# Kernel tuning notes

Measured on AMD Instinct MI355X. Metric: run time of the kernel, lower is better.

Reference implementation:

```python
import jax, jax.numpy as jnp
import numpy as np

D = 11           # num_classes + 1 (embedding dim)
HL = 7           # window height = 1 + 2*H_PAD
WL = 7           # window width  = 1 + 2*W_PAD
PAD = 3
MAXH, MAXW = 30, 30
FF = 64          # dim_feedforward
EPS = 1e-5       # LayerNorm eps (torch default)
PAD_VALUE = 0.0


def setup_inputs() -> dict:
    key = jax.random.key(0)
    ks = jax.random.split(key, 6)
    N, C, H, W = 1, 10, 16, 16
    s = 0.1
    return {
        "x": jax.random.uniform(ks[0], (N, C, H, W), jnp.float32),
        "Wqkv": jax.random.normal(ks[1], (3 * D, D), jnp.float32) * s,  # in_proj_weight
        "Wo": jax.random.normal(ks[2], (D, D), jnp.float32) * s,        # out_proj.weight
        "W1": jax.random.normal(ks[3], (FF, D), jnp.float32) * s,       # linear1.weight
        "W2": jax.random.normal(ks[4], (D, FF), jnp.float32) * s,       # linear2.weight
        "ln1_w": jnp.ones((D,), jnp.float32),                           # norm1.weight (bias=False)
        "ln2_w": jnp.ones((D,), jnp.float32),                           # norm2.weight (bias=False)
    }


def _layer_norm(x, w):
    m = jnp.mean(x, axis=-1, keepdims=True)
    v = jnp.mean(jnp.square(x - m), axis=-1, keepdims=True)
    return (x - m) / jnp.sqrt(v + EPS) * w


def _encoder_layer(x, Wqkv, Wo, W1, W2, ln1_w, ln2_w):
    # x: [B, S, D]; post-norm, 1 head, no biases, eval mode (dropout off)
    qkv = x @ Wqkv.T
    q, k, v = jnp.split(qkv, 3, axis=-1)
    scale = 1.0 / jnp.sqrt(jnp.float32(D))
    attn = jax.nn.softmax(jnp.einsum('bqd,bkd->bqk', q, k) * scale, axis=-1)
    sa = jnp.einsum('bqk,bkd->bqd', attn, v) @ Wo.T
    x = _layer_norm(x + sa, ln1_w)
    ff = jax.nn.relu(x @ W1.T) @ W2.T
    return _layer_norm(x + ff, ln2_w)


def reference(x, Wqkv, Wo, W1, W2, ln1_w, ln2_w):
    N, C, H, W = x.shape
    C1 = C + 1
    # mask channel: 1 in the padded border, 0 inside
    mask = jnp.pad(jnp.zeros((N, 1, H, W), x.dtype),
                   ((0, 0), (0, 0), (PAD, PAD), (PAD, PAD)), constant_values=1.0)
    xp = jnp.pad(x, ((0, 0), (0, 0), (PAD, PAD), (PAD, PAD)), constant_values=PAD_VALUE)
    xp = jnp.concatenate([xp, mask], axis=1)            # [N, C+1, H+6, W+6]
    win = jnp.stack([xp[:, :, i:i + H, j:j + W]
                     for i in range(HL) for j in range(WL)], axis=-1)  # [N, C1, H, W, 49]
    win = jnp.transpose(win, (0, 2, 3, 1, 4))           # [N, H, W, C1, 49]
    win = win.reshape(N * H * W * C1, HL, WL)
    # embed window into max_height x max_width canvas (rest = pad_value)
    canvas = jnp.full((N * H * W * C1, MAXH, MAXW), PAD_VALUE, x.dtype)
    canvas = canvas.at[:, :HL, :WL].set(win)
    seq = canvas.reshape(N * H * W, C1, MAXH * MAXW).transpose(0, 2, 1)  # [B, S=900, D=11]
    out = _encoder_layer(seq, Wqkv, Wo, W1, W2, ln1_w, ln2_w)
    return out.transpose(0, 2, 1)[:, :-1]               # [B, C, 900]
```

## Files before the change

### kernel.cpp

```cpp
#include <hip/hip_runtime.h>


#define D 11
#define ROWP 12
#define NW 49
#define NWP 52
#define NR 50
#define SEQ 900
#define FFD 64
#define CIN 10
#define NB 256
#define TPB 576
#define NRD (NR * D)

__device__ __forceinline__ float dot12(const float4* a, const float4* b) {
    float4 s = make_float4(0.f, 0.f, 0.f, 0.f);
    #pragma unroll
    for (int i = 0; i < 3; ++i) {
        float4 x = a[i], y = b[i];
        s.x += x.x * y.x; s.y += x.y * y.y; s.z += x.z * y.z; s.w += x.w * y.w;
    }
    return s.x + s.y + s.z + s.w;
}

__global__ __launch_bounds__(TPB) void pve_kernel(
    const float* __restrict__ gx,
    const float* __restrict__ gWqkv,
    const float* __restrict__ gWo,
    const float* __restrict__ gW1,
    const float* __restrict__ gW2,
    const float* __restrict__ gln1,
    const float* __restrict__ gln2,
    float* __restrict__ out)
{
    __shared__ __align__(16) float sQ[33 * ROWP];
    __shared__ __align__(16) float sWo[D * ROWP];
    __shared__ __align__(16) float sW1[FFD * ROWP];
    __shared__ __align__(16) float sW2[D * FFD];
    __shared__ float sln1[D], sln2[D];
    __shared__ __align__(16) float sSeq[NR][ROWP];
    __shared__ __align__(16) float sK[NW][ROWP];
    __shared__ __align__(16) float sVt[D][NWP];
    __shared__ __align__(16) float sQr[NR][ROWP];
    __shared__ __align__(16) float sE[NR][NWP];
    __shared__ __align__(16) float sNum[NR][ROWP];
    __shared__ float sDen[NR];
    __shared__ __align__(16) float sX1[NR][ROWP];
    __shared__ __align__(16) float sX1n[NR][ROWP];
    __shared__ __align__(16) float sH[NR][FFD];
    __shared__ __align__(16) float sY[NR][ROWP];
    __shared__ __align__(16) float sR[NR][ROWP];

    const int tid = threadIdx.x;
    const int b = blockIdx.x;
    const int h = b >> 4;
    const int w = b & 15;

    const int rd = tid;
    const int r = rd / D;
    const int d = rd - r * D;

    for (int i = tid; i < 33 * ROWP; i += TPB) {
        const int rr = i / ROWP, cc = i - rr * ROWP;
        sQ[i] = (cc < D) ? gWqkv[rr * D + cc] : 0.f;
    }
    for (int i = tid; i < D * ROWP; i += TPB) {
        const int rr = i / ROWP, cc = i - rr * ROWP;
        sWo[i] = (cc < D) ? gWo[rr * D + cc] : 0.f;
    }
    for (int i = tid; i < FFD * ROWP; i += TPB) {
        const int rr = i / ROWP, cc = i - rr * ROWP;
        sW1[i] = (cc < D) ? gW1[rr * D + cc] : 0.f;
    }
    for (int i = tid; i < D * FFD; i += TPB) sW2[i] = gW2[i];
    if (tid < D) { sln1[tid] = gln1[tid]; sln2[tid] = gln2[tid]; }

    if (rd < NRD) {
        float val = 0.0f;
        if (r < NW) {
            const int i = r / 7, j = r - (r / 7) * 7;
            const int y = h + i, xx = w + j;
            const bool inter = (y >= 3) && (y < 19) && (xx >= 3) && (xx < 19);
            const int base = inter ? ((y - 3) * 16 + (xx - 3)) : 0;
            if (d < CIN) val = inter ? gx[d * 256 + base] : 0.0f;
            else         val = inter ? 0.0f : 1.0f;
        }
        sSeq[r][d] = val;
        if (d == CIN) sSeq[r][D] = 0.f;
    }
    __syncthreads();

    if (rd < NRD) {
        const float4* sv = (const float4*)&sSeq[r][0];
        const float aq = dot12(sv, (const float4*)&sQ[d * ROWP]);
        const float ak = dot12(sv, (const float4*)&sQ[(D + d) * ROWP]);
        const float av = dot12(sv, (const float4*)&sQ[(2 * D + d) * ROWP]);
        sQr[r][d] = aq;
        if (d == CIN) sQr[r][D] = 0.f;
        if (r < NW) { sK[r][d] = ak; sVt[d][r] = av;
                      if (d == CIN) sK[r][D] = 0.f; }
        else { sVt[d][NW] = 0.f; sVt[d][NW + 1] = 0.f; sVt[d][NW + 2] = 0.f; }
    }
    __syncthreads();

    {
        const float scale = 0.30151134457776363f;
        #pragma unroll
        for (int k = 0; k < 5; ++k) {
            const int idx = tid + k * TPB;
            if (idx < NR * NWP) {
                const int rr = idx / NWP;
                const int tt = idx - rr * NWP;
                float e = 0.f;
                if (tt < NW) {
                    const float s = dot12((const float4*)&sQr[rr][0],
                                          (const float4*)&sK[tt][0]);
                    e = __expf(s * scale);
                }
                sE[rr][tt] = e;
            }
        }
    }
    __syncthreads();

    if (rd < NRD) {
        const float4* ev = (const float4*)&sE[r][0];
        const float4* vv = (const float4*)&sVt[d][0];
        float4 an = make_float4(0.f, 0.f, 0.f, 0.f);
        float4 ad = make_float4(0.f, 0.f, 0.f, 0.f);
        #pragma unroll
        for (int i = 0; i < 13; ++i) {
            const float4 e = ev[i], v = vv[i];
            an.x += e.x * v.x; an.y += e.y * v.y;
            an.z += e.z * v.z; an.w += e.w * v.w;
            ad.x += e.x; ad.y += e.y; ad.z += e.z; ad.w += e.w;
        }
        sNum[r][d] = an.x + an.y + an.z + an.w;
        if (d == CIN) sNum[r][D] = 0.f;
        if (d == 0) sDen[r] = 851.0f + ad.x + ad.y + ad.z + ad.w;
    }
    __syncthreads();

    if (rd < NRD) {
        const float acc = dot12((const float4*)&sNum[r][0],
                                (const float4*)&sWo[d * ROWP]);
        sX1[r][d] = sSeq[r][d] + acc / sDen[r];
        if (d == CIN) sX1[r][D] = 0.f;
    }
    __syncthreads();

    if (rd < NRD) {
        const float4* xv = (const float4*)&sX1[r][0];
        float4 s4 = make_float4(0.f, 0.f, 0.f, 0.f);
        float4 q4 = make_float4(0.f, 0.f, 0.f, 0.f);
        #pragma unroll
        for (int i = 0; i < 3; ++i) {
            const float4 x = xv[i];
            s4.x += x.x; s4.y += x.y; s4.z += x.z; s4.w += x.w;
            q4.x += x.x * x.x; q4.y += x.y * x.y;
            q4.z += x.z * x.z; q4.w += x.w * x.w;
        }
        const float sum = s4.x + s4.y + s4.z + s4.w;
        const float sq  = q4.x + q4.y + q4.z + q4.w;
        const float m   = sum * (1.0f / 11.0f);
        const float var = sq * (1.0f / 11.0f) - m * m;
        sX1n[r][d] = (sX1[r][d] - m) * rsqrtf(var + 1e-5f) * sln1[d];
        if (d == CIN) sX1n[r][D] = 0.f;
    }
    __syncthreads();

    #pragma unroll
    for (int k = 0; k < 6; ++k) {
        const int idx = tid + k * TPB;
        if (idx < NR * FFD) {
            const int rr = idx >> 6;
            const int ff = idx & 63;
            const float acc = dot12((const float4*)&sX1n[rr][0],
                                    (const float4*)&sW1[ff * ROWP]);
            sH[rr][ff] = fmaxf(acc, 0.0f);
        }
    }
    __syncthreads();

    if (rd < NRD) {
        const float4* hv = (const float4*)&sH[r][0];
        const float4* wv = (const float4*)&sW2[d * FFD];
        float4 a4 = make_float4(0.f, 0.f, 0.f, 0.f);
        #pragma unroll
        for (int i = 0; i < 16; ++i) {
            const float4 hh = hv[i], ww = wv[i];
            a4.x += hh.x * ww.x; a4.y += hh.y * ww.y;
            a4.z += hh.z * ww.z; a4.w += hh.w * ww.w;
        }
        sY[r][d] = sX1n[r][d] + a4.x + a4.y + a4.z + a4.w;
        if (d == CIN) sY[r][D] = 0.f;
    }
    __syncthreads();

    if (rd < NRD) {
        const float4* yv = (const float4*)&sY[r][0];
        float4 s4 = make_float4(0.f, 0.f, 0.f, 0.f);
        float4 q4 = make_float4(0.f, 0.f, 0.f, 0.f);
        #pragma unroll
        for (int i = 0; i < 3; ++i) {
            const float4 y = yv[i];
            s4.x += y.x; s4.y += y.y; s4.z += y.z; s4.w += y.w;
            q4.x += y.x * y.x; q4.y += y.y * y.y;
            q4.z += y.z * y.z; q4.w += y.w * y.w;
        }
        const float sum = s4.x + s4.y + s4.z + s4.w;
        const float sq  = q4.x + q4.y + q4.z + q4.w;
        const float m   = sum * (1.0f / 11.0f);
        const float var = sq * (1.0f / 11.0f) - m * m;
        sR[r][d] = (sY[r][d] - m) * rsqrtf(var + 1e-5f) * sln2[d];
    }
    __syncthreads();

    float4* ob4 = (float4*)(out + b * (CIN * SEQ));
    #pragma unroll
    for (int k = 0; k < 4; ++k) {
        const int qi = tid + k * TPB;
        if (qi < 2250) {
            const int c  = qi / 225;
            const int s0 = (qi - c * 225) * 4;
            float4 v4;
            float* pv = (float*)&v4;
            #pragma unroll
            for (int u = 0; u < 4; ++u) {
                const int s = s0 + u;
                const int i = s / 30;
                const int j = s - i * 30;
                pv[u] = (i < 7 && j < 7) ? sR[i * 7 + j][c] : sR[NW][c];
            }
            ob4[qi] = v4;
        }
    }
}

extern "C" void kernel_launch(void* const* d_in, const int* in_sizes, int n_in,
                              void* d_out, int out_size, void* d_ws, size_t ws_size,
                              hipStream_t stream) {
    (void)in_sizes; (void)n_in; (void)out_size; (void)d_ws; (void)ws_size;
    const float* x    = (const float*)d_in[0];
    const float* Wqkv = (const float*)d_in[1];
    const float* Wo   = (const float*)d_in[2];
    const float* W1   = (const float*)d_in[3];
    const float* W2   = (const float*)d_in[4];
    const float* ln1  = (const float*)d_in[5];
    const float* ln2  = (const float*)d_in[6];
    pve_kernel<<<NB, TPB, 0, stream>>>(x, Wqkv, Wo, W1, W2, ln1, ln2,
                                       (float*)d_out);
}
```

Before: 80.08 us.

## Split compute and output scatter into two kernels via workspace buffer

The fused kernel now writes only the 50 distinct per-row results per channel into a compact workspace table. A second, fully parallel kernel expands that table into the 900-position output with coalesced float4 stores. This decouples the large, mostly redundant output write from the 256-block compute kernel so it can use the whole GPU. The cost is an extra kernel launch and a round trip through global memory.

```diff
diff --git a/kernel.cpp b/kernel.cpp
--- a/kernel.cpp
+++ b/kernel.cpp
@@ -12,6 +12,7 @@
 #define NB 256
 #define TPB 576
 #define NRD (NR * D)
+#define TROW 52
 
 __device__ __forceinline__ float dot12(const float4* a, const float4* b) {
     float4 s = make_float4(0.f, 0.f, 0.f, 0.f);
@@ -23,7 +24,7 @@
     return s.x + s.y + s.z + s.w;
 }
 
-__global__ __launch_bounds__(TPB) void pve_kernel(
+__global__ __launch_bounds__(TPB) void pve_rows(
     const float* __restrict__ gx,
     const float* __restrict__ gWqkv,
     const float* __restrict__ gWo,
@@ -31,7 +32,7 @@
     const float* __restrict__ gW2,
     const float* __restrict__ gln1,
     const float* __restrict__ gln2,
-    float* __restrict__ out)
+    float* __restrict__ T)
 {
     __shared__ __align__(16) float sQ[33 * ROWP];
     __shared__ __align__(16) float sWo[D * ROWP];
@@ -49,7 +50,6 @@
     __shared__ __align__(16) float sX1n[NR][ROWP];
     __shared__ __align__(16) float sH[NR][FFD];
     __shared__ __align__(16) float sY[NR][ROWP];
-    __shared__ __align__(16) float sR[NR][ROWP];
 
     const int tid = threadIdx.x;
     const int b = blockIdx.x;
@@ -212,35 +212,39 @@
         const float sq  = q4.x + q4.y + q4.z + q4.w;
         const float m   = sum * (1.0f / 11.0f);
         const float var = sq * (1.0f / 11.0f) - m * m;
-        sR[r][d] = (sY[r][d] - m) * rsqrtf(var + 1e-5f) * sln2[d];
-    }
-    __syncthreads();
-
-    float4* ob4 = (float4*)(out + b * (CIN * SEQ));
+        const float val = (sY[r][d] - m) * rsqrtf(var + 1e-5f) * sln2[d];
+        if (d < CIN)
+            T[(b * CIN + d) * TROW + r] = val;
+    }
+}
+
+__global__ __launch_bounds__(256) void pve_write(
+    const float* __restrict__ T,
+    float4* __restrict__ out4)
+{
+    const int flat = blockIdx.x * 256 + threadIdx.x;
+    const int b   = flat / 2250;
+    const int rem = flat - b * 2250;
+    const int c   = rem / 225;
+    const int s0  = (rem - c * 225) * 4;
+    const float* tb = T + (b * CIN + c) * TROW;
+    float4 v4;
+    float* pv = (float*)&v4;
     #pragma unroll
-    for (int k = 0; k < 4; ++k) {
-        const int qi = tid + k * TPB;
-        if (qi < 2250) {
-            const int c  = qi / 225;
-            const int s0 = (qi - c * 225) * 4;
-            float4 v4;
-            float* pv = (float*)&v4;
-            #pragma unroll
-            for (int u = 0; u < 4; ++u) {
-                const int s = s0 + u;
-                const int i = s / 30;
-                const int j = s - i * 30;
-                pv[u] = (i < 7 && j < 7) ? sR[i * 7 + j][c] : sR[NW][c];
-            }
-            ob4[qi] = v4;
-        }
-    }
+    for (int u = 0; u < 4; ++u) {
+        const int s = s0 + u;
+        const int i = s / 30;
+        const int j = s - i * 30;
+        const int row = (i < 7 && j < 7) ? (i * 7 + j) : NW;
+        pv[u] = tb[row];
+    }
+    out4[flat] = v4;
 }
 
 extern "C" void kernel_launch(void* const* d_in, const int* in_sizes, int n_in,
                               void* d_out, int out_size, void* d_ws, size_t ws_size,
                               hipStream_t stream) {
-    (void)in_sizes; (void)n_in; (void)out_size; (void)d_ws; (void)ws_size;
+    (void)in_sizes; (void)n_in; (void)out_size; (void)ws_size;
     const float* x    = (const float*)d_in[0];
     const float* Wqkv = (const float*)d_in[1];
     const float* Wo   = (const float*)d_in[2];
@@ -248,6 +252,7 @@
     const float* W2   = (const float*)d_in[4];
     const float* ln1  = (const float*)d_in[5];
     const float* ln2  = (const float*)d_in[6];
-    pve_kernel<<<NB, TPB, 0, stream>>>(x, Wqkv, Wo, W1, W2, ln1, ln2,
-                                       (float*)d_out);
-}
+    float* T = (float*)d_ws;
+    pve_rows<<<NB, TPB, 0, stream>>>(x, Wqkv, Wo, W1, W2, ln1, ln2, T);
+    pve_write<<<576000 / 256, 256, 0, stream>>>(T, (float4*)d_out);
+}
```

New measurement: 81.29 us. Within noise of the previous version (+1.5%).
